# Kernel tuning notes

Measured on AMD Instinct MI355X. Metric: run time of the kernel, lower is better.

Reference implementation:

```python
import jax, jax.numpy as jnp
import numpy as np

T_IN, T_OUT = 16, 25          # in_length, out_length
B, K = 4096, 32               # heroes, neighbors per hero
N = B * K                     # total neighbor tracks
ENC, DEC, DYN, EMB = 64, 128, 32, 32


def _lrelu(x):
    return jnp.where(x >= 0, x, 0.1 * x)


def _lstm(x, Wih, Whh, bih, bhh, hidden):
    """PyTorch-convention LSTM (gate order i,f,g,o). x: [T, B, D]. Returns (all_h [T,B,H], last_h [B,H])."""
    z = jnp.zeros((x.shape[1], hidden), x.dtype)

    def step(carry, xt):
        h, c = carry
        g = xt @ Wih.T + bih + h @ Whh.T + bhh
        i, f, gg, o = jnp.split(g, 4, axis=-1)
        c = jax.nn.sigmoid(f) * c + jax.nn.sigmoid(i) * jnp.tanh(gg)
        h = jax.nn.sigmoid(o) * jnp.tanh(c)
        return (h, c), h

    (h, c), hs = jax.lax.scan(step, (z, z), x)
    return hs, h


def setup_inputs() -> dict:
    key = jax.random.key(0)
    ks = jax.random.split(key, 20)
    p = lambda k, s: jax.random.normal(k, s, jnp.float32) * 0.1
    return {
        "hist": jax.random.normal(ks[0], (T_IN, B, 2), jnp.float32),
        "nbrs": jax.random.normal(ks[1], (T_IN, N, 2), jnp.float32),
        "Wip": p(ks[2], (EMB, 2)), "bip": p(ks[3], (EMB,)),
        "Wih_e": p(ks[4], (4 * ENC, EMB)), "Whh_e": p(ks[5], (4 * ENC, ENC)),
        "bih_e": p(ks[6], (4 * ENC,)), "bhh_e": p(ks[7], (4 * ENC,)),
        "Wdyn": p(ks[8], (DYN, ENC)), "bdyn": p(ks[9], (DYN,)),
        "Wnbr": p(ks[10], (ENC, 2 * T_IN)), "bnbr": p(ks[11], (ENC,)),
        "Wih_d": p(ks[12], (4 * DEC, 2 * DYN)), "Whh_d": p(ks[13], (4 * DEC, DEC)),
        "bih_d": p(ks[14], (4 * DEC,)), "bhh_d": p(ks[15], (4 * DEC,)),
        "Wop": p(ks[16], (2, DEC)), "bop": p(ks[17], (2,)),
        # index_division flattened: neighbor j belongs to hero segment_ids[j] (sorted, K per hero)
        "segment_ids": jnp.repeat(jnp.arange(B, dtype=jnp.int32), K),
    }


def reference(hist, nbrs, Wip, bip, Wih_e, Whh_e, bih_e, bhh_e, Wdyn, bdyn,
              Wnbr, bnbr, Wih_d, Whh_d, bih_d, bhh_d, Wop, bop, segment_ids):
    # --- encode ego history ---
    emb = _lrelu(hist @ Wip.T + bip)                       # [T,B,EMB]
    _, h_enc = _lstm(emb, Wih_e, Whh_e, bih_e, bhh_e, ENC)  # [B,ENC]
    hist_e = _lrelu(h_enc @ Wdyn.T + bdyn)                 # [B,DYN]

    # --- relative neighbor tracks + ragged segment-max pooling ---
    relative = hist[:, segment_ids, :] - nbrs              # [T,N,2]  (hero_repeated gather)
    rela = jnp.transpose(relative, (1, 0, 2)).reshape(N, 2 * T_IN)  # permute(1,0,2).view(-1,2*in_length)
    rela_enc = _lrelu(rela @ Wnbr.T + bnbr)                # [N,ENC]
    scene = jax.ops.segment_max(rela_enc, segment_ids, num_segments=B)  # fused per-group max
    scene = _lrelu(scene @ Wdyn.T + bdyn)                  # [B,DYN]

    # --- decode ---
    enc = jnp.concatenate([hist_e, scene], axis=1)         # [B,2*DYN]
    dec_in = jnp.broadcast_to(enc, (T_OUT, B, 2 * DYN))    # unsqueeze(0).repeat(out_length,1,1)
    h_dec, _ = _lstm(dec_in, Wih_d, Whh_d, bih_d, bhh_d, DEC)  # [T_OUT,B,DEC]
    fut = h_dec @ Wop.T + bop                              # [T_OUT,B,2]
    # outputActivation: with 2 output dims (muX,muY only) it is the identity
    return fut
```

## Files before the change

kernel.cpp:

```cpp
#include <hip/hip_runtime.h>
#include <hip/hip_bf16.h>

#define T_IN   16
#define T_OUT  25
#define BHERO  4096
#define K_NBR  32
#define N_NBR  (BHERO * K_NBR)
#define ENC    64
#define DEC    128
#define DYN    32
#define EMB    32

#define EROW   104
#define DROW   136
#define RROW   40
#define SLABE  (16 * EROW * 2)
#define SLABD  (16 * DROW * 2)

#define OFF_RELA   56576
#define OFF_PMAX   97536
#define OFF_ENC    113152
#define OFF_WOP    117504
#define OFF_WIP    118528
#define OFF_BIP    118784
#define OFF_BOP    118912
#define LDS_TOTAL  118928

#define L2E 1.44269504f

typedef __attribute__((ext_vector_type(8))) short bf16x8;
typedef __attribute__((ext_vector_type(4))) float f32x4;

__device__ __forceinline__ float lrelu(float x) { return x >= 0.f ? x : 0.1f * x; }
__device__ __forceinline__ float rcpf(float x)  { return __builtin_amdgcn_rcpf(x); }
__device__ __forceinline__ float ex2(float x)   { return __builtin_amdgcn_exp2f(x); }
__device__ __forceinline__ float sigm2(float x) { return rcpf(1.f + ex2(-x)); }
__device__ __forceinline__ float tanh2(float x) { return fmaf(2.f, rcpf(1.f + ex2(-x)), -1.f); }
__device__ __forceinline__ float tanhc(float c) {
    return fmaf(2.f, rcpf(1.f + ex2(-2.f * L2E * c)), -1.f);
}
__device__ __forceinline__ short f2bf(float x) {
    __hip_bfloat16 b = __float2bfloat16(x);
    short s; __builtin_memcpy(&s, &b, 2); return s;
}
__device__ __forceinline__ unsigned pk2(float lo, float hi) {
    __hip_bfloat162 p = __float22bfloat162_rn(make_float2(lo, hi));
    unsigned u; __builtin_memcpy(&u, &p, 4); return u;
}
__device__ __forceinline__ bf16x8 mk_frag(float4 f0, float4 f1) {
    uint4 v = { pk2(f0.x, f0.y), pk2(f0.z, f0.w), pk2(f1.x, f1.y), pk2(f1.z, f1.w) };
    bf16x8 r; __builtin_memcpy(&r, &v, 16); return r;
}
__device__ __forceinline__ bf16x8 mk_frag_s(float4 f0, float4 f1, float s) {
    uint4 v = { pk2(f0.x*s, f0.y*s), pk2(f0.z*s, f0.w*s), pk2(f1.x*s, f1.y*s), pk2(f1.z*s, f1.w*s) };
    bf16x8 r; __builtin_memcpy(&r, &v, 16); return r;
}
__device__ __forceinline__ float bf2f(short s) {
    return __uint_as_float(((unsigned)(unsigned short)s) << 16);
}

__global__ __launch_bounds__(512, 2) void highway_fused(
    const float* __restrict__ hist,  const float* __restrict__ nbrs,
    const float* __restrict__ Wip,   const float* __restrict__ bip,
    const float* __restrict__ WihE,  const float* __restrict__ WhhE,
    const float* __restrict__ bihE,  const float* __restrict__ bhhE,
    const float* __restrict__ Wdyn,  const float* __restrict__ bdyn,
    const float* __restrict__ Wnbr,  const float* __restrict__ bnbr,
    const float* __restrict__ WihD,  const float* __restrict__ WhhD,
    const float* __restrict__ bihD,  const float* __restrict__ bhhD,
    const float* __restrict__ Wop,   const float* __restrict__ bop,
    const int*   __restrict__ seg,
    float* __restrict__ fut)
{
    __shared__ __align__(16) char lds_raw[LDS_TOTAL];
    auto slab   = (short (*)[16][EROW])  lds_raw;
    auto rela   = (short (*)[RROW])     (lds_raw + OFF_RELA);
    auto pmax   = (float (*)[ENC])      (lds_raw + OFF_PMAX);
    auto hist_s = (short (*)[16][DROW])  lds_raw;
    auto enc_s  = (float (*)[68])       (lds_raw + OFF_ENC);
    auto wop_s  = (float (*)[DEC])      (lds_raw + OFF_WOP);
    auto wip_s  = (float (*)[2])        (lds_raw + OFF_WIP);
    auto bip_s  = (float*)              (lds_raw + OFF_BIP);
    auto bop_s  = (float*)              (lds_raw + OFF_BOP);

    const int b0  = blockIdx.x * 16;
    const int n0  = blockIdx.x * 512;
    const int tid = threadIdx.x;
    const int w = tid >> 6, l = tid & 63, r = l & 15, lg = l >> 4;

    if (tid < EMB) {
        wip_s[tid][0] = Wip[2 * tid];
        wip_s[tid][1] = Wip[2 * tid + 1];
        bip_s[tid]    = bip[tid];
    }
    if (tid < 2 * DEC) wop_s[tid >> 7][tid & 127] = Wop[tid];
    if (tid < 2)       bop_s[tid] = bop[tid];
    for (int i = tid; i < 16 * ENC; i += 512) slab[0][i >> 6][32 + (i & 63)] = 0;

    bf16x8 BfE[4][3];
    float  biasE[4];
    bf16x8 BfN[2];
    float  biasn[2] = {0.f, 0.f};
    if (tid < 256) {
        #pragma unroll
        for (int j = 0; j < 4; ++j) {
            const float sj  = (j == 2) ? (2.f * L2E) : L2E;
            const int   col = j * ENC + w * 16 + r;
            biasE[j] = (bihE[col] + bhhE[col]) * sj;
            #pragma unroll
            for (int c = 0; c < 3; ++c) {
                const float* src = (c == 0) ? (WihE + (size_t)col * EMB + 8 * lg)
                                            : (WhhE + (size_t)col * ENC + (c - 1) * 32 + 8 * lg);
                BfE[j][c] = mk_frag_s(*(const float4*)src, *(const float4*)(src + 4), sj);
            }
        }
    } else {
        const int i = w - 4;
        const int ct0 = (i & 1) * 2;
        #pragma unroll
        for (int cc2 = 0; cc2 < 2; ++cc2) {
            const int col = (ct0 + cc2) * 16 + r;
            biasn[cc2] = bnbr[col];
            const float* src = Wnbr + (size_t)col * (2 * T_IN) + 8 * lg;
            BfN[cc2] = mk_frag(*(const float4*)src, *(const float4*)(src + 4));
        }
    }
    __syncthreads();

    if (tid < 256) {
        const int t = tid >> 4, m = tid & 15;
        float2 hv = *(const float2*)&hist[((size_t)t * BHERO + b0 + m) * 2];
        #pragma unroll
        for (int jb = 0; jb < 4; ++jb) {
            float e[8];
            #pragma unroll
            for (int q = 0; q < 8; ++q) {
                int j = jb * 8 + q;
                e[q] = lrelu(hv.x * wip_s[j][0] + hv.y * wip_s[j][1] + bip_s[j]);
            }
            uint4 v = { pk2(e[0],e[1]), pk2(e[2],e[3]), pk2(e[4],e[5]), pk2(e[6],e[7]) };
            __builtin_memcpy(&slab[t][m][jb * 8], &v, 16);
        }
    } else {
        const int x = tid - 256;
        const int n  = x & 31;
        const int ts = x >> 5;
        const int hb = seg[n0 + n];
        float2 h0 = *(const float2*)&hist[((size_t)ts * BHERO + hb) * 2];
        float2 v0 = *(const float2*)&nbrs[((size_t)ts * N_NBR + n0 + n) * 2];
        float2 h1 = *(const float2*)&hist[((size_t)(ts + 8) * BHERO + hb) * 2];
        float2 v1 = *(const float2*)&nbrs[((size_t)(ts + 8) * N_NBR + n0 + n) * 2];
        unsigned* dst = (unsigned*)&rela[n][0];
        dst[ts]     = pk2(h0.x - v0.x, h0.y - v0.y);
        dst[ts + 8] = pk2(h1.x - v1.x, h1.y - v1.y);
    }
    f32x4 cstE = {0.f, 0.f, 0.f, 0.f};
    __syncthreads();

    {
        const char* rbase = lds_raw + (size_t)r * (EROW * 2);
        char*       wbase = lds_raw + SLABE + (size_t)(4 * lg) * (EROW * 2) + (size_t)(32 + w * 16 + r) * 2;
        const int   x = tid - 256;
        #pragma unroll 1
        for (int t = 0; t < T_IN; ++t) {
            if (tid < 256) {
                const short* rp = (const short*)rbase;
                bf16x8 a0 = *(const bf16x8*)(rp + (0 + lg) * 8);
                bf16x8 a1 = *(const bf16x8*)(rp + (4 + lg) * 8);
                bf16x8 a2 = *(const bf16x8*)(rp + (8 + lg) * 8);
                f32x4 acc[4];
                #pragma unroll
                for (int j = 0; j < 4; ++j) {
                    f32x4 aA = (f32x4){biasE[j], biasE[j], biasE[j], biasE[j]};
                    f32x4 aB = (f32x4){0.f, 0.f, 0.f, 0.f};
                    aA = __builtin_amdgcn_mfma_f32_16x16x32_bf16(a0, BfE[j][0], aA, 0, 0, 0);
                    aB = __builtin_amdgcn_mfma_f32_16x16x32_bf16(a1, BfE[j][1], aB, 0, 0, 0);
                    aA = __builtin_amdgcn_mfma_f32_16x16x32_bf16(a2, BfE[j][2], aA, 0, 0, 0);
                    acc[j] = aA + aB;
                }
                float hq[4];
                #pragma unroll
                for (int q = 0; q < 4; ++q) {
                    float ii = sigm2(acc[0][q]);
                    float ff = sigm2(acc[1][q]);
                    float gg = tanh2(acc[2][q]);
                    float oo = sigm2(acc[3][q]);
                    float cc = fmaf(ff, cstE[q], ii * gg);
                    cstE[q] = cc;
                    hq[q] = oo * tanhc(cc);
                }
                unsigned u01 = pk2(hq[0], hq[1]), u23 = pk2(hq[2], hq[3]);
                short* wp = (short*)wbase;
                wp[0 * EROW] = (short)u01; wp[1 * EROW] = (short)(u01 >> 16);
                wp[2 * EROW] = (short)u23; wp[3 * EROW] = (short)(u23 >> 16);
            } else {
                if (t < T_IN - 1) {
                    const int n  = 32 * (t + 1) + (x & 31);
                    const int ts = x >> 5;
                    const int hb = seg[n0 + n];
                    float2 h0 = *(const float2*)&hist[((size_t)ts * BHERO + hb) * 2];
                    float2 v0 = *(const float2*)&nbrs[((size_t)ts * N_NBR + n0 + n) * 2];
                    float2 h1 = *(const float2*)&hist[((size_t)(ts + 8) * BHERO + hb) * 2];
                    float2 v1 = *(const float2*)&nbrs[((size_t)(ts + 8) * N_NBR + n0 + n) * 2];
                    unsigned* dst = (unsigned*)&rela[n][0];
                    dst[ts]     = pk2(h0.x - v0.x, h0.y - v0.y);
                    dst[ts + 8] = pk2(h1.x - v1.x, h1.y - v1.y);
                }
                const int i  = w - 4;
                const int rt = 2 * t + (i >> 1);
                const int ct0 = (i & 1) * 2;
                bf16x8 a = *(const bf16x8*)&rela[rt * 16 + r][8 * lg];
                #pragma unroll
                for (int cc2 = 0; cc2 < 2; ++cc2) {
                    f32x4 acc = {biasn[cc2], biasn[cc2], biasn[cc2], biasn[cc2]};
                    acc = __builtin_amdgcn_mfma_f32_16x16x32_bf16(a, BfN[cc2], acc, 0, 0, 0);
                    float m4 = fmaxf(fmaxf(acc[0], acc[1]), fmaxf(acc[2], acc[3]));
                    m4 = fmaxf(m4, __shfl_xor(m4, 16));
                    m4 = fmaxf(m4, __shfl_xor(m4, 32));
                    if (l < 16) pmax[rt][(ct0 + cc2) * 16 + r] = m4;
                }
            }
            __syncthreads();
            rbase += SLABE; wbase += SLABE;
        }
    }

    #pragma unroll
    for (int it = 0; it < 2; ++it) {
        const int s = tid + 512 * it;
        const int m = s >> 6, col = s & 63;
        const float* wd = Wdyn + (size_t)(col & 31) * ENC;
        float a = bdyn[col & 31];
        if (col < 32) {
            const short* hp = &slab[T_IN][m][32];
            #pragma unroll
            for (int kb = 0; kb < 8; ++kb) {
                bf16x8 hv = *(const bf16x8*)(hp + kb * 8);
                #pragma unroll
                for (int e = 0; e < 8; ++e)
                    a = fmaf(bf2f(hv[e]), wd[kb * 8 + e], a);
            }
        } else {
            #pragma unroll
            for (int kb = 0; kb < 16; ++kb) {
                float4 p0 = *(const float4*)&pmax[2 * m][kb * 4];
                float4 p1 = *(const float4*)&pmax[2 * m + 1][kb * 4];
                a = fmaf(lrelu(fmaxf(p0.x, p1.x)), wd[kb * 4 + 0], a);
                a = fmaf(lrelu(fmaxf(p0.y, p1.y)), wd[kb * 4 + 1], a);
                a = fmaf(lrelu(fmaxf(p0.z, p1.z)), wd[kb * 4 + 2], a);
                a = fmaf(lrelu(fmaxf(p0.w, p1.w)), wd[kb * 4 + 3], a);
            }
        }
        enc_s[m][col] = lrelu(a);
    }
    for (int i = tid; i < 16 * DROW; i += 512) ((short*)hist_s)[i] = 0;
    __syncthreads();

    const int u0 = w * 16;
    bf16x8 BfD[4][4];
    float  biasD[4];
    float  sjD[4];
    #pragma unroll
    for (int j = 0; j < 4; ++j) {
        const float sj  = (j == 2) ? (2.f * L2E) : L2E;
        const int   col = j * DEC + u0 + r;
        sjD[j]   = sj;
        biasD[j] = (bihD[col] + bhhD[col]) * sj;
        #pragma unroll
        for (int c = 0; c < 4; ++c) {
            const float* src = WhhD + (size_t)col * DEC + c * 32 + 8 * lg;
            BfD[j][c] = mk_frag_s(*(const float4*)src, *(const float4*)(src + 4), sj);
        }
    }
    f32x4 xwf[4];
    {
        bf16x8 aE[2];
        #pragma unroll
        for (int c = 0; c < 2; ++c) {
            float4 f0 = *(const float4*)&enc_s[r][c * 32 + 8 * lg];
            float4 f1 = *(const float4*)&enc_s[r][c * 32 + 8 * lg + 4];
            aE[c] = mk_frag(f0, f1);
        }
        #pragma unroll
        for (int j = 0; j < 4; ++j) {
            const int col = j * DEC + u0 + r;
            f32x4 a = {biasD[j], biasD[j], biasD[j], biasD[j]};
            #pragma unroll
            for (int c = 0; c < 2; ++c) {
                const float* src = WihD + (size_t)col * (2 * DYN) + c * 32 + 8 * lg;
                a = __builtin_amdgcn_mfma_f32_16x16x32_bf16(
                        aE[c], mk_frag_s(*(const float4*)src, *(const float4*)(src + 4), sjD[j]),
                        a, 0, 0, 0);
            }
            xwf[j] = a;
        }
    }

    f32x4 cst = {0.f, 0.f, 0.f, 0.f};
    {
        const char* rbase = lds_raw + (size_t)r * (DROW * 2);
        char*       wbase = lds_raw + SLABD + (size_t)(4 * lg) * (DROW * 2) + (size_t)(u0 + r) * 2;
        #pragma unroll 1
        for (int t = 0; t < T_OUT; ++t) {
            const short* rp = (const short*)rbase;
            bf16x8 a_[4];
            #pragma unroll
            for (int c = 0; c < 4; ++c)
                a_[c] = *(const bf16x8*)(rp + (4 * c + lg) * 8);
            f32x4 acc[4];
            #pragma unroll
            for (int j = 0; j < 4; ++j) {
                f32x4 aA = xwf[j];
                f32x4 aB = (f32x4){0.f, 0.f, 0.f, 0.f};
                aA = __builtin_amdgcn_mfma_f32_16x16x32_bf16(a_[0], BfD[j][0], aA, 0, 0, 0);
                aB = __builtin_amdgcn_mfma_f32_16x16x32_bf16(a_[1], BfD[j][1], aB, 0, 0, 0);
                aA = __builtin_amdgcn_mfma_f32_16x16x32_bf16(a_[2], BfD[j][2], aA, 0, 0, 0);
                aB = __builtin_amdgcn_mfma_f32_16x16x32_bf16(a_[3], BfD[j][3], aB, 0, 0, 0);
                acc[j] = aA + aB;
            }
            float hq[4];
            #pragma unroll
            for (int q = 0; q < 4; ++q) {
                float ii = sigm2(acc[0][q]);
                float ff = sigm2(acc[1][q]);
                float gg = tanh2(acc[2][q]);
                float oo = sigm2(acc[3][q]);
                float cc = fmaf(ff, cst[q], ii * gg);
                cst[q] = cc;
                hq[q] = oo * tanhc(cc);
            }
            unsigned u01 = pk2(hq[0], hq[1]), u23 = pk2(hq[2], hq[3]);
            short* wp = (short*)wbase;
            wp[0 * DROW] = (short)u01; wp[1 * DROW] = (short)(u01 >> 16);
            wp[2 * DROW] = (short)u23; wp[3 * DROW] = (short)(u23 >> 16);
            __syncthreads();
            rbase += SLABD; wbase += SLABD;
        }
    }

    if (tid < T_OUT * 16) {
        const int t = tid >> 4, m = tid & 15;
        const short* hp = &hist_s[t + 1][m][0];
        float o0 = bop_s[0], o1 = bop_s[1];
        #pragma unroll
        for (int ub = 0; ub < DEC / 8; ++ub) {
            bf16x8 hv = *(const bf16x8*)(hp + ub * 8);
            #pragma unroll
            for (int e = 0; e < 8; ++e) {
                float h = bf2f(hv[e]);
                o0 = fmaf(h, wop_s[0][ub * 8 + e], o0);
                o1 = fmaf(h, wop_s[1][ub * 8 + e], o1);
            }
        }
        *(float2*)(fut + ((size_t)t * BHERO + b0 + m) * 2) = make_float2(o0, o1);
    }
}

extern "C" void kernel_launch(void* const* d_in, const int* in_sizes, int n_in,
                              void* d_out, int out_size, void* d_ws, size_t ws_size,
                              hipStream_t stream) {
    (void)d_ws; (void)ws_size; (void)in_sizes; (void)n_in; (void)out_size;
    const float* hist  = (const float*)d_in[0];
    const float* nbrs  = (const float*)d_in[1];
    const float* Wip   = (const float*)d_in[2];
    const float* bip   = (const float*)d_in[3];
    const float* Wih_e = (const float*)d_in[4];
    const float* Whh_e = (const float*)d_in[5];
    const float* bih_e = (const float*)d_in[6];
    const float* bhh_e = (const float*)d_in[7];
    const float* Wdyn  = (const float*)d_in[8];
    const float* bdyn  = (const float*)d_in[9];
    const float* Wnbr  = (const float*)d_in[10];
    const float* bnbr  = (const float*)d_in[11];
    const float* Wih_d = (const float*)d_in[12];
    const float* Whh_d = (const float*)d_in[13];
    const float* bih_d = (const float*)d_in[14];
    const float* bhh_d = (const float*)d_in[15];
    const float* Wop   = (const float*)d_in[16];
    const float* bop   = (const float*)d_in[17];
    const int*   seg   = (const int*)d_in[18];
    float* fut = (float*)d_out;

    hipLaunchKernelGGL(highway_fused, dim3(BHERO / 16), dim3(512), 0, stream,
                       hist, nbrs, Wip, bip, Wih_e, Whh_e, bih_e, bhh_e, Wdyn, bdyn,
                       Wnbr, bnbr, Wih_d, Whh_d, bih_d, bhh_d, Wop, bop, seg, fut);
}
```

Before: 63.58 us.

## Software-pipeline neighbor loads with double-buffered rela and lighter LDS-only barriers

Neighbor relative-track loads are now issued two timesteps ahead into registers, and the segment id three steps ahead. The rela LDS buffer shrinks to a two-slot ring indexed by timestep parity, so global load latency overlaps the encoder LSTM steps instead of stalling each iteration. __syncthreads is replaced by an inline asm that waits only on lgkmcnt before s_barrier, so barriers no longer wait for outstanding global loads. This costs extra registers, and correctness depends on the parity buffer not being overwritten before it is read.

```diff
diff --git a/kernel.cpp b/kernel.cpp
--- a/kernel.cpp
+++ b/kernel.cpp
@@ -39,10 +39,6 @@
 __device__ __forceinline__ float tanhc(float c) {
     return fmaf(2.f, rcpf(1.f + ex2(-2.f * L2E * c)), -1.f);
 }
-__device__ __forceinline__ short f2bf(float x) {
-    __hip_bfloat16 b = __float2bfloat16(x);
-    short s; __builtin_memcpy(&s, &b, 2); return s;
-}
 __device__ __forceinline__ unsigned pk2(float lo, float hi) {
     __hip_bfloat162 p = __float22bfloat162_rn(make_float2(lo, hi));
     unsigned u; __builtin_memcpy(&u, &p, 4); return u;
@@ -57,6 +53,9 @@
 }
 __device__ __forceinline__ float bf2f(short s) {
     return __uint_as_float(((unsigned)(unsigned short)s) << 16);
+}
+__device__ __forceinline__ void bar_lgkm() {
+    asm volatile("s_waitcnt lgkmcnt(0)\n\ts_barrier" ::: "memory");
 }
 
 __global__ __launch_bounds__(512, 2) void highway_fused(
@@ -74,7 +73,7 @@
 {
     __shared__ __align__(16) char lds_raw[LDS_TOTAL];
     auto slab   = (short (*)[16][EROW])  lds_raw;
-    auto rela   = (short (*)[RROW])     (lds_raw + OFF_RELA);
+    auto rela2  = (short (*)[32][RROW]) (lds_raw + OFF_RELA);
     auto pmax   = (float (*)[ENC])      (lds_raw + OFF_PMAX);
     auto hist_s = (short (*)[16][DROW])  lds_raw;
     auto enc_s  = (float (*)[68])       (lds_raw + OFF_ENC);
@@ -125,8 +124,10 @@
             BfN[cc2] = mk_frag(*(const float4*)src, *(const float4*)(src + 4));
         }
     }
-    __syncthreads();
-
+    bar_lgkm();
+
+    float2 c_h0, c_v0, c_h1, c_v1;
+    int    sg_c = 0;
     if (tid < 256) {
         const int t = tid >> 4, m = tid & 15;
         float2 hv = *(const float2*)&hist[((size_t)t * BHERO + b0 + m) * 2];
@@ -142,25 +143,38 @@
             __builtin_memcpy(&slab[t][m][jb * 8], &v, 16);
         }
     } else {
-        const int x = tid - 256;
-        const int n  = x & 31;
-        const int ts = x >> 5;
-        const int hb = seg[n0 + n];
-        float2 h0 = *(const float2*)&hist[((size_t)ts * BHERO + hb) * 2];
-        float2 v0 = *(const float2*)&nbrs[((size_t)ts * N_NBR + n0 + n) * 2];
-        float2 h1 = *(const float2*)&hist[((size_t)(ts + 8) * BHERO + hb) * 2];
-        float2 v1 = *(const float2*)&nbrs[((size_t)(ts + 8) * N_NBR + n0 + n) * 2];
-        unsigned* dst = (unsigned*)&rela[n][0];
-        dst[ts]     = pk2(h0.x - v0.x, h0.y - v0.y);
-        dst[ts + 8] = pk2(h1.x - v1.x, h1.y - v1.y);
+        const int x    = tid - 256;
+        const int nloc = x & 31;
+        const int ts   = x >> 5;
+        {
+            const int hb = seg[n0 + nloc];
+            float2 h0 = *(const float2*)&hist[((size_t)ts * BHERO + hb) * 2];
+            float2 v0 = *(const float2*)&nbrs[((size_t)ts * N_NBR + n0 + nloc) * 2];
+            float2 h1 = *(const float2*)&hist[((size_t)(ts + 8) * BHERO + hb) * 2];
+            float2 v1 = *(const float2*)&nbrs[((size_t)(ts + 8) * N_NBR + n0 + nloc) * 2];
+            unsigned* dst = (unsigned*)&rela2[0][nloc][0];
+            dst[ts]     = pk2(h0.x - v0.x, h0.y - v0.y);
+            dst[ts + 8] = pk2(h1.x - v1.x, h1.y - v1.y);
+        }
+        {
+            const int n  = 32 + nloc;
+            const int hb = seg[n0 + n];
+            c_h0 = *(const float2*)&hist[((size_t)ts * BHERO + hb) * 2];
+            c_v0 = *(const float2*)&nbrs[((size_t)ts * N_NBR + n0 + n) * 2];
+            c_h1 = *(const float2*)&hist[((size_t)(ts + 8) * BHERO + hb) * 2];
+            c_v1 = *(const float2*)&nbrs[((size_t)(ts + 8) * N_NBR + n0 + n) * 2];
+        }
+        sg_c = seg[n0 + 64 + nloc];
     }
     f32x4 cstE = {0.f, 0.f, 0.f, 0.f};
-    __syncthreads();
+    bar_lgkm();
 
     {
         const char* rbase = lds_raw + (size_t)r * (EROW * 2);
         char*       wbase = lds_raw + SLABE + (size_t)(4 * lg) * (EROW * 2) + (size_t)(32 + w * 16 + r) * 2;
-        const int   x = tid - 256;
+        const int   x    = tid - 256;
+        const int   nloc = x & 31;
+        const int   ts   = x >> 5;
         #pragma unroll 1
         for (int t = 0; t < T_IN; ++t) {
             if (tid < 256) {
@@ -194,22 +208,26 @@
                 wp[0 * EROW] = (short)u01; wp[1 * EROW] = (short)(u01 >> 16);
                 wp[2 * EROW] = (short)u23; wp[3 * EROW] = (short)(u23 >> 16);
             } else {
+                float2 n_h0, n_v0, n_h1, n_v1;
+                int    sg_n = 0;
+                if (t < T_IN - 2) {
+                    const int n  = 32 * (t + 2) + nloc;
+                    const int hb = sg_c;
+                    n_h0 = *(const float2*)&hist[((size_t)ts * BHERO + hb) * 2];
+                    n_v0 = *(const float2*)&nbrs[((size_t)ts * N_NBR + n0 + n) * 2];
+                    n_h1 = *(const float2*)&hist[((size_t)(ts + 8) * BHERO + hb) * 2];
+                    n_v1 = *(const float2*)&nbrs[((size_t)(ts + 8) * N_NBR + n0 + n) * 2];
+                }
+                if (t < T_IN - 3) sg_n = seg[n0 + 32 * (t + 3) + nloc];
                 if (t < T_IN - 1) {
-                    const int n  = 32 * (t + 1) + (x & 31);
-                    const int ts = x >> 5;
-                    const int hb = seg[n0 + n];
-                    float2 h0 = *(const float2*)&hist[((size_t)ts * BHERO + hb) * 2];
-                    float2 v0 = *(const float2*)&nbrs[((size_t)ts * N_NBR + n0 + n) * 2];
-                    float2 h1 = *(const float2*)&hist[((size_t)(ts + 8) * BHERO + hb) * 2];
-                    float2 v1 = *(const float2*)&nbrs[((size_t)(ts + 8) * N_NBR + n0 + n) * 2];
-                    unsigned* dst = (unsigned*)&rela[n][0];
-                    dst[ts]     = pk2(h0.x - v0.x, h0.y - v0.y);
-                    dst[ts + 8] = pk2(h1.x - v1.x, h1.y - v1.y);
+                    unsigned* dst = (unsigned*)&rela2[(t + 1) & 1][nloc][0];
+                    dst[ts]     = pk2(c_h0.x - c_v0.x, c_h0.y - c_v0.y);
+                    dst[ts + 8] = pk2(c_h1.x - c_v1.x, c_h1.y - c_v1.y);
                 }
-                const int i  = w - 4;
-                const int rt = 2 * t + (i >> 1);
+                const int i   = w - 4;
+                const int lrt = i >> 1;
                 const int ct0 = (i & 1) * 2;
-                bf16x8 a = *(const bf16x8*)&rela[rt * 16 + r][8 * lg];
+                bf16x8 a = *(const bf16x8*)&rela2[t & 1][lrt * 16 + r][8 * lg];
                 #pragma unroll
                 for (int cc2 = 0; cc2 < 2; ++cc2) {
                     f32x4 acc = {biasn[cc2], biasn[cc2], biasn[cc2], biasn[cc2]};
@@ -217,10 +235,12 @@
                     float m4 = fmaxf(fmaxf(acc[0], acc[1]), fmaxf(acc[2], acc[3]));
                     m4 = fmaxf(m4, __shfl_xor(m4, 16));
                     m4 = fmaxf(m4, __shfl_xor(m4, 32));
-                    if (l < 16) pmax[rt][(ct0 + cc2) * 16 + r] = m4;
+                    if (l < 16) pmax[2 * t + lrt][(ct0 + cc2) * 16 + r] = m4;
                 }
-            }
-            __syncthreads();
+                c_h0 = n_h0; c_v0 = n_v0; c_h1 = n_h1; c_v1 = n_v1;
+                sg_c = sg_n;
+            }
+            bar_lgkm();
             rbase += SLABE; wbase += SLABE;
         }
     }
@@ -254,7 +274,7 @@
         enc_s[m][col] = lrelu(a);
     }
     for (int i = tid; i < 16 * DROW; i += 512) ((short*)hist_s)[i] = 0;
-    __syncthreads();
+    bar_lgkm();
 
     const int u0 = w * 16;
     bf16x8 BfD[4][4];
@@ -333,7 +353,7 @@
             short* wp = (short*)wbase;
             wp[0 * DROW] = (short)u01; wp[1 * DROW] = (short)(u01 >> 16);
             wp[2 * DROW] = (short)u23; wp[3 * DROW] = (short)(u23 >> 16);
-            __syncthreads();
+            bar_lgkm();
             rbase += SLABD; wbase += SLABD;
         }
     }
```

Result: no change. 64.21 us (+1.0%).

## Halve heroes per block to 8 with 256 threads and ring-buffered LDS state

Applied to the files above, without the earlier changes.

Each block now handles 8 heroes with 256 threads instead of 16 heroes with 512, which doubles the grid to 512 blocks. The 16-row MFMA tiles are filled by duplicating each hero's rows, so half of the matrix work is redundant. Each wave computes two unit slices and keeps only its own. Full per-timestep LDS slabs are replaced by double-buffered rings, cutting LDS use from about 119KB to 66KB so more blocks can be resident per CU. Barriers now use a custom lgkmcnt wait plus s_barrier. The trade is more grid parallelism and occupancy against duplicated MFMA work and more registers per thread.

```diff
diff --git a/kernel.cpp b/kernel.cpp
--- a/kernel.cpp
+++ b/kernel.cpp
@@ -10,21 +10,22 @@
 #define DEC    128
 #define DYN    32
 #define EMB    32
-
-#define EROW   104
+#define HEROES 8
+
 #define DROW   136
+#define HROW   72
+#define EMROW  40
 #define RROW   40
-#define SLABE  (16 * EROW * 2)
-#define SLABD  (16 * DROW * 2)
-
-#define OFF_RELA   56576
-#define OFF_PMAX   97536
-#define OFF_ENC    113152
-#define OFF_WOP    117504
-#define OFF_WIP    118528
-#define OFF_BIP    118784
-#define OFF_BOP    118912
-#define LDS_TOTAL  118928
+
+#define OFF_HRING  20480
+#define OFF_RELA   25088
+#define OFF_PMAX   27648
+#define OFF_ENC    59904
+#define OFF_WOP    64256
+#define OFF_WIP    65280
+#define OFF_BIP    65536
+#define OFF_BOP    65664
+#define LDS_TOTAL  65680
 
 #define L2E 1.44269504f
 
@@ -58,8 +59,11 @@
 __device__ __forceinline__ float bf2f(short s) {
     return __uint_as_float(((unsigned)(unsigned short)s) << 16);
 }
-
-__global__ __launch_bounds__(512, 2) void highway_fused(
+__device__ __forceinline__ void bar_lgkm() {
+    asm volatile("s_waitcnt lgkmcnt(0)\n\ts_barrier" ::: "memory");
+}
+
+__global__ __launch_bounds__(256, 2) void highway_fused(
     const float* __restrict__ hist,  const float* __restrict__ nbrs,
     const float* __restrict__ Wip,   const float* __restrict__ bip,
     const float* __restrict__ WihE,  const float* __restrict__ WhhE,
@@ -73,50 +77,58 @@
     float* __restrict__ fut)
 {
     __shared__ __align__(16) char lds_raw[LDS_TOTAL];
-    auto slab   = (short (*)[16][EROW])  lds_raw;
-    auto rela   = (short (*)[RROW])     (lds_raw + OFF_RELA);
-    auto pmax   = (float (*)[ENC])      (lds_raw + OFF_PMAX);
-    auto hist_s = (short (*)[16][DROW])  lds_raw;
-    auto enc_s  = (float (*)[68])       (lds_raw + OFF_ENC);
-    auto wop_s  = (float (*)[DEC])      (lds_raw + OFF_WOP);
-    auto wip_s  = (float (*)[2])        (lds_raw + OFF_WIP);
-    auto bip_s  = (float*)              (lds_raw + OFF_BIP);
-    auto bop_s  = (float*)              (lds_raw + OFF_BOP);
-
-    const int b0  = blockIdx.x * 16;
-    const int n0  = blockIdx.x * 512;
+    auto ring   = (short (*)[16][DROW])   lds_raw;
+    auto hhist  = (short (*)[HEROES][DEC])(lds_raw + 8704);
+    auto embs   = (short (*)[16][EMROW])  lds_raw;
+    auto hring  = (short (*)[16][HROW])  (lds_raw + OFF_HRING);
+    auto rela   = (short (*)[16][RROW])  (lds_raw + OFF_RELA);
+    auto pmax   = (float (*)[ENC])       (lds_raw + OFF_PMAX);
+    auto enc_s  = (float (*)[68])        (lds_raw + OFF_ENC);
+    auto wop_s  = (float (*)[DEC])       (lds_raw + OFF_WOP);
+    auto wip_s  = (float (*)[2])         (lds_raw + OFF_WIP);
+    auto bip_s  = (float*)               (lds_raw + OFF_BIP);
+    auto bop_s  = (float*)               (lds_raw + OFF_BOP);
+
+    const int b0  = blockIdx.x * HEROES;
+    const int n0  = blockIdx.x * (HEROES * K_NBR);
     const int tid = threadIdx.x;
     const int w = tid >> 6, l = tid & 63, r = l & 15, lg = l >> 4;
+    const int ubsel = lg >> 1;
+    const int hgrp  = (lg & 1) * 4;
+    const int unit  = 32 * w + 16 * ubsel + r;
 
     if (tid < EMB) {
         wip_s[tid][0] = Wip[2 * tid];
         wip_s[tid][1] = Wip[2 * tid + 1];
         bip_s[tid]    = bip[tid];
     }
-    if (tid < 2 * DEC) wop_s[tid >> 7][tid & 127] = Wop[tid];
-    if (tid < 2)       bop_s[tid] = bop[tid];
-    for (int i = tid; i < 16 * ENC; i += 512) slab[0][i >> 6][32 + (i & 63)] = 0;
-
-    bf16x8 BfE[4][3];
-    float  biasE[4];
+    wop_s[tid >> 7][tid & 127] = Wop[tid];
+    if (tid < 2) bop_s[tid] = bop[tid];
+    for (int i = tid; i < 16 * HROW; i += 256) ((short*)hring[0])[i] = 0;
+    bar_lgkm();
+
+    bf16x8 BfE[2][4][3];
+    float  biasE[2][4];
     bf16x8 BfN[2];
     float  biasn[2] = {0.f, 0.f};
-    if (tid < 256) {
-        #pragma unroll
-        for (int j = 0; j < 4; ++j) {
-            const float sj  = (j == 2) ? (2.f * L2E) : L2E;
-            const int   col = j * ENC + w * 16 + r;
-            biasE[j] = (bihE[col] + bhhE[col]) * sj;
-            #pragma unroll
-            for (int c = 0; c < 3; ++c) {
-                const float* src = (c == 0) ? (WihE + (size_t)col * EMB + 8 * lg)
-                                            : (WhhE + (size_t)col * ENC + (c - 1) * 32 + 8 * lg);
-                BfE[j][c] = mk_frag_s(*(const float4*)src, *(const float4*)(src + 4), sj);
+    if (tid < 128) {
+        #pragma unroll
+        for (int ub = 0; ub < 2; ++ub) {
+            #pragma unroll
+            for (int j = 0; j < 4; ++j) {
+                const float sj  = (j == 2) ? (2.f * L2E) : L2E;
+                const int   col = j * ENC + 32 * w + 16 * ub + r;
+                biasE[ub][j] = (bihE[col] + bhhE[col]) * sj;
+                #pragma unroll
+                for (int c = 0; c < 3; ++c) {
+                    const float* src = (c == 0) ? (WihE + (size_t)col * EMB + 8 * lg)
+                                                : (WhhE + (size_t)col * ENC + (c - 1) * 32 + 8 * lg);
+                    BfE[ub][j][c] = mk_frag_s(*(const float4*)src, *(const float4*)(src + 4), sj);
+                }
             }
         }
     } else {
-        const int i = w - 4;
-        const int ct0 = (i & 1) * 2;
+        const int ct0 = 2 * (w - 2);
         #pragma unroll
         for (int cc2 = 0; cc2 < 2; ++cc2) {
             const int col = (ct0 + cc2) * 16 + r;
@@ -125,114 +137,114 @@
             BfN[cc2] = mk_frag(*(const float4*)src, *(const float4*)(src + 4));
         }
     }
-    __syncthreads();
-
-    if (tid < 256) {
-        const int t = tid >> 4, m = tid & 15;
+    {
+        const int task = tid >> 1;
+        const int t = task >> 3, m = task & 7;
+        const int j0 = (tid & 1) * 16;
         float2 hv = *(const float2*)&hist[((size_t)t * BHERO + b0 + m) * 2];
         #pragma unroll
-        for (int jb = 0; jb < 4; ++jb) {
+        for (int jb = 0; jb < 2; ++jb) {
             float e[8];
             #pragma unroll
             for (int q = 0; q < 8; ++q) {
-                int j = jb * 8 + q;
+                int j = j0 + jb * 8 + q;
                 e[q] = lrelu(hv.x * wip_s[j][0] + hv.y * wip_s[j][1] + bip_s[j]);
             }
             uint4 v = { pk2(e[0],e[1]), pk2(e[2],e[3]), pk2(e[4],e[5]), pk2(e[6],e[7]) };
-            __builtin_memcpy(&slab[t][m][jb * 8], &v, 16);
-        }
-    } else {
-        const int x = tid - 256;
-        const int n  = x & 31;
-        const int ts = x >> 5;
+            __builtin_memcpy(&embs[t][m][j0 + jb * 8], &v, 16);
+            __builtin_memcpy(&embs[t][m + 8][j0 + jb * 8], &v, 16);
+        }
+    }
+    if (tid >= 128) {
+        const int x  = tid - 128;
+        const int n  = x & 15;
+        const int ts = x >> 4;
         const int hb = seg[n0 + n];
         float2 h0 = *(const float2*)&hist[((size_t)ts * BHERO + hb) * 2];
         float2 v0 = *(const float2*)&nbrs[((size_t)ts * N_NBR + n0 + n) * 2];
         float2 h1 = *(const float2*)&hist[((size_t)(ts + 8) * BHERO + hb) * 2];
         float2 v1 = *(const float2*)&nbrs[((size_t)(ts + 8) * N_NBR + n0 + n) * 2];
-        unsigned* dst = (unsigned*)&rela[n][0];
+        unsigned* dst = (unsigned*)&rela[0][n][0];
         dst[ts]     = pk2(h0.x - v0.x, h0.y - v0.y);
         dst[ts + 8] = pk2(h1.x - v1.x, h1.y - v1.y);
     }
     f32x4 cstE = {0.f, 0.f, 0.f, 0.f};
-    __syncthreads();
-
-    {
-        const char* rbase = lds_raw + (size_t)r * (EROW * 2);
-        char*       wbase = lds_raw + SLABE + (size_t)(4 * lg) * (EROW * 2) + (size_t)(32 + w * 16 + r) * 2;
-        const int   x = tid - 256;
-        #pragma unroll 1
-        for (int t = 0; t < T_IN; ++t) {
-            if (tid < 256) {
-                const short* rp = (const short*)rbase;
-                bf16x8 a0 = *(const bf16x8*)(rp + (0 + lg) * 8);
-                bf16x8 a1 = *(const bf16x8*)(rp + (4 + lg) * 8);
-                bf16x8 a2 = *(const bf16x8*)(rp + (8 + lg) * 8);
-                f32x4 acc[4];
+    bar_lgkm();
+
+    #pragma unroll 1
+    for (int t = 0; t < T_IN; ++t) {
+        const int cur = t & 1, nxt = cur ^ 1;
+        if (tid < 128) {
+            bf16x8 a0 = *(const bf16x8*)&embs[t][r][8 * lg];
+            bf16x8 a1 = *(const bf16x8*)&hring[cur][r][8 * lg];
+            bf16x8 a2 = *(const bf16x8*)&hring[cur][r][32 + 8 * lg];
+            f32x4 acc[2][4];
+            #pragma unroll
+            for (int ub = 0; ub < 2; ++ub) {
                 #pragma unroll
                 for (int j = 0; j < 4; ++j) {
-                    f32x4 aA = (f32x4){biasE[j], biasE[j], biasE[j], biasE[j]};
+                    f32x4 aA = (f32x4){biasE[ub][j], biasE[ub][j], biasE[ub][j], biasE[ub][j]};
                     f32x4 aB = (f32x4){0.f, 0.f, 0.f, 0.f};
-                    aA = __builtin_amdgcn_mfma_f32_16x16x32_bf16(a0, BfE[j][0], aA, 0, 0, 0);
-                    aB = __builtin_amdgcn_mfma_f32_16x16x32_bf16(a1, BfE[j][1], aB, 0, 0, 0);
-                    aA = __builtin_amdgcn_mfma_f32_16x16x32_bf16(a2, BfE[j][2], aA, 0, 0, 0);
-                    acc[j] = aA + aB;
+                    aA = __builtin_amdgcn_mfma_f32_16x16x32_bf16(a0, BfE[ub][j][0], aA, 0, 0, 0);
+                    aB = __builtin_amdgcn_mfma_f32_16x16x32_bf16(a1, BfE[ub][j][1], aB, 0, 0, 0);
+                    aA = __builtin_amdgcn_mfma_f32_16x16x32_bf16(a2, BfE[ub][j][2], aA, 0, 0, 0);
+                    acc[ub][j] = aA + aB;
                 }
-                float hq[4];
-                #pragma unroll
-                for (int q = 0; q < 4; ++q) {
-                    float ii = sigm2(acc[0][q]);
-                    float ff = sigm2(acc[1][q]);
-                    float gg = tanh2(acc[2][q]);
-                    float oo = sigm2(acc[3][q]);
-                    float cc = fmaf(ff, cstE[q], ii * gg);
-                    cstE[q] = cc;
-                    hq[q] = oo * tanhc(cc);
-                }
-                unsigned u01 = pk2(hq[0], hq[1]), u23 = pk2(hq[2], hq[3]);
-                short* wp = (short*)wbase;
-                wp[0 * EROW] = (short)u01; wp[1 * EROW] = (short)(u01 >> 16);
-                wp[2 * EROW] = (short)u23; wp[3 * EROW] = (short)(u23 >> 16);
-            } else {
-                if (t < T_IN - 1) {
-                    const int n  = 32 * (t + 1) + (x & 31);
-                    const int ts = x >> 5;
-                    const int hb = seg[n0 + n];
-                    float2 h0 = *(const float2*)&hist[((size_t)ts * BHERO + hb) * 2];
-                    float2 v0 = *(const float2*)&nbrs[((size_t)ts * N_NBR + n0 + n) * 2];
-                    float2 h1 = *(const float2*)&hist[((size_t)(ts + 8) * BHERO + hb) * 2];
-                    float2 v1 = *(const float2*)&nbrs[((size_t)(ts + 8) * N_NBR + n0 + n) * 2];
-                    unsigned* dst = (unsigned*)&rela[n][0];
-                    dst[ts]     = pk2(h0.x - v0.x, h0.y - v0.y);
-                    dst[ts + 8] = pk2(h1.x - v1.x, h1.y - v1.y);
-                }
-                const int i  = w - 4;
-                const int rt = 2 * t + (i >> 1);
-                const int ct0 = (i & 1) * 2;
-                bf16x8 a = *(const bf16x8*)&rela[rt * 16 + r][8 * lg];
-                #pragma unroll
-                for (int cc2 = 0; cc2 < 2; ++cc2) {
-                    f32x4 acc = {biasn[cc2], biasn[cc2], biasn[cc2], biasn[cc2]};
-                    acc = __builtin_amdgcn_mfma_f32_16x16x32_bf16(a, BfN[cc2], acc, 0, 0, 0);
-                    float m4 = fmaxf(fmaxf(acc[0], acc[1]), fmaxf(acc[2], acc[3]));
-                    m4 = fmaxf(m4, __shfl_xor(m4, 16));
-                    m4 = fmaxf(m4, __shfl_xor(m4, 32));
-                    if (l < 16) pmax[rt][(ct0 + cc2) * 16 + r] = m4;
-                }
-            }
-            __syncthreads();
-            rbase += SLABE; wbase += SLABE;
-        }
+            }
+            f32x4 g0 = (ubsel == 0) ? acc[0][0] : acc[1][0];
+            f32x4 g1 = (ubsel == 0) ? acc[0][1] : acc[1][1];
+            f32x4 g2 = (ubsel == 0) ? acc[0][2] : acc[1][2];
+            f32x4 g3 = (ubsel == 0) ? acc[0][3] : acc[1][3];
+            const int ue = 32 * w + 16 * ubsel + r;
+            #pragma unroll
+            for (int q = 0; q < 4; ++q) {
+                float ii = sigm2(g0[q]);
+                float ff = sigm2(g1[q]);
+                float gg = tanh2(g2[q]);
+                float oo = sigm2(g3[q]);
+                float cc = fmaf(ff, cstE[q], ii * gg);
+                cstE[q] = cc;
+                short hb16 = f2bf(oo * tanhc(cc));
+                hring[nxt][hgrp + q][ue]     = hb16;
+                hring[nxt][hgrp + q + 8][ue] = hb16;
+            }
+        } else {
+            const int x = tid - 128;
+            if (t < T_IN - 1) {
+                const int n  = 16 * (t + 1) + (x & 15);
+                const int ts = x >> 4;
+                const int hb = seg[n0 + n];
+                float2 h0 = *(const float2*)&hist[((size_t)ts * BHERO + hb) * 2];
+                float2 v0 = *(const float2*)&nbrs[((size_t)ts * N_NBR + n0 + n) * 2];
+                float2 h1 = *(const float2*)&hist[((size_t)(ts + 8) * BHERO + hb) * 2];
+                float2 v1 = *(const float2*)&nbrs[((size_t)(ts + 8) * N_NBR + n0 + n) * 2];
+                unsigned* dst = (unsigned*)&rela[(t + 1) & 1][x & 15][0];
+                dst[ts]     = pk2(h0.x - v0.x, h0.y - v0.y);
+                dst[ts + 8] = pk2(h1.x - v1.x, h1.y - v1.y);
+            }
+            const int ct0 = 2 * (w - 2);
+            bf16x8 a = *(const bf16x8*)&rela[t & 1][r][8 * lg];
+            #pragma unroll
+            for (int cc2 = 0; cc2 < 2; ++cc2) {
+                f32x4 acc = {biasn[cc2], biasn[cc2], biasn[cc2], biasn[cc2]};
+                acc = __builtin_amdgcn_mfma_f32_16x16x32_bf16(a, BfN[cc2], acc, 0, 0, 0);
+                float m4 = fmaxf(fmaxf(acc[0], acc[1]), fmaxf(acc[2], acc[3]));
+                m4 = fmaxf(m4, __shfl_xor(m4, 16));
+                m4 = fmaxf(m4, __shfl_xor(m4, 32));
+                if (l < 16) pmax[t][(ct0 + cc2) * 16 + r] = m4;
+            }
+        }
+        bar_lgkm();
     }
 
     #pragma unroll
     for (int it = 0; it < 2; ++it) {
-        const int s = tid + 512 * it;
+        const int s = tid + 256 * it;
         const int m = s >> 6, col = s & 63;
         const float* wd = Wdyn + (size_t)(col & 31) * ENC;
         float a = bdyn[col & 31];
         if (col < 32) {
-            const short* hp = &slab[T_IN][m][32];
+            const short* hp = &hring[T_IN & 1 ^ 0][m][0];
             #pragma unroll
             for (int kb = 0; kb < 8; ++kb) {
                 bf16x8 hv = *(const bf16x8*)(hp + kb * 8);
@@ -251,28 +263,30 @@
                 a = fmaf(lrelu(fmaxf(p0.w, p1.w)), wd[kb * 4 + 3], a);
             }
         }
-        enc_s[m][col] = lrelu(a);
-    }
-    for (int i = tid; i < 16 * DROW; i += 512) ((short*)hist_s)[i] = 0;
-    __syncthreads();
-
-    const int u0 = w * 16;
-    bf16x8 BfD[4][4];
-    float  biasD[4];
-    float  sjD[4];
+        float av = lrelu(a);
+        enc_s[m][col]     = av;
+        enc_s[m + 8][col] = av;
+    }
+    for (int i = tid; i < 16 * DROW; i += 256) ((short*)ring[0])[i] = 0;
+    bar_lgkm();
+
+    bf16x8 BfD[2][4][4];
+    float  biasD[2][4];
     #pragma unroll
-    for (int j = 0; j < 4; ++j) {
-        const float sj  = (j == 2) ? (2.f * L2E) : L2E;
-        const int   col = j * DEC + u0 + r;
-        sjD[j]   = sj;
-        biasD[j] = (bihD[col] + bhhD[col]) * sj;
-        #pragma unroll
-        for (int c = 0; c < 4; ++c) {
-            const float* src = WhhD + (size_t)col * DEC + c * 32 + 8 * lg;
-            BfD[j][c] = mk_frag_s(*(const float4*)src, *(const float4*)(src + 4), sj);
-        }
-    }
-    f32x4 xwf[4];
+    for (int ub = 0; ub < 2; ++ub) {
+        #pragma unroll
+        for (int j = 0; j < 4; ++j) {
+            const float sj  = (j == 2) ? (2.f * L2E) : L2E;
+            const int   col = j * DEC + 32 * w + 16 * ub + r;
+            biasD[ub][j] = (bihD[col] + bhhD[col]) * sj;
+            #pragma unroll
+            for (int c = 0; c < 4; ++c) {
+                const float* src = WhhD + (size_t)col * DEC + c * 32 + 8 * lg;
+                BfD[ub][j][c] = mk_frag_s(*(const float4*)src, *(const float4*)(src + 4), sj);
+            }
+        }
+    }
+    f32x4 xwf[2][4];
     {
         bf16x8 aE[2];
         #pragma unroll
@@ -282,65 +296,70 @@
             aE[c] = mk_frag(f0, f1);
         }
         #pragma unroll
-        for (int j = 0; j < 4; ++j) {
-            const int col = j * DEC + u0 + r;
-            f32x4 a = {biasD[j], biasD[j], biasD[j], biasD[j]};
-            #pragma unroll
-            for (int c = 0; c < 2; ++c) {
-                const float* src = WihD + (size_t)col * (2 * DYN) + c * 32 + 8 * lg;
-                a = __builtin_amdgcn_mfma_f32_16x16x32_bf16(
-                        aE[c], mk_frag_s(*(const float4*)src, *(const float4*)(src + 4), sjD[j]),
-                        a, 0, 0, 0);
-            }
-            xwf[j] = a;
+        for (int ub = 0; ub < 2; ++ub) {
+            #pragma unroll
+            for (int j = 0; j < 4; ++j) {
+                const float sj  = (j == 2) ? (2.f * L2E) : L2E;
+                const int   col = j * DEC + 32 * w + 16 * ub + r;
+                f32x4 a = {biasD[ub][j], biasD[ub][j], biasD[ub][j], biasD[ub][j]};
+                #pragma unroll
+                for (int c = 0; c < 2; ++c) {
+                    const float* src = WihD + (size_t)col * (2 * DYN) + c * 32 + 8 * lg;
+                    a = __builtin_amdgcn_mfma_f32_16x16x32_bf16(
+                            aE[c], mk_frag_s(*(const float4*)src, *(const float4*)(src + 4), sj),
+                            a, 0, 0, 0);
+                }
+                xwf[ub][j] = a;
+            }
         }
     }
 
     f32x4 cst = {0.f, 0.f, 0.f, 0.f};
-    {
-        const char* rbase = lds_raw + (size_t)r * (DROW * 2);
-        char*       wbase = lds_raw + SLABD + (size_t)(4 * lg) * (DROW * 2) + (size_t)(u0 + r) * 2;
-        #pragma unroll 1
-        for (int t = 0; t < T_OUT; ++t) {
-            const short* rp = (const short*)rbase;
-            bf16x8 a_[4];
-            #pragma unroll
-            for (int c = 0; c < 4; ++c)
-                a_[c] = *(const bf16x8*)(rp + (4 * c + lg) * 8);
-            f32x4 acc[4];
+    #pragma unroll 1
+    for (int t = 0; t < T_OUT; ++t) {
+        const int cur = t & 1, nxt = cur ^ 1;
+        const short* rp = &ring[cur][r][0];
+        bf16x8 a_[4];
+        #pragma unroll
+        for (int c = 0; c < 4; ++c)
+            a_[c] = *(const bf16x8*)(rp + (4 * c + lg) * 8);
+        f32x4 acc[2][4];
+        #pragma unroll
+        for (int ub = 0; ub < 2; ++ub) {
             #pragma unroll
             for (int j = 0; j < 4; ++j) {
-                f32x4 aA = xwf[j];
+                f32x4 aA = xwf[ub][j];
                 f32x4 aB = (f32x4){0.f, 0.f, 0.f, 0.f};
-                aA = __builtin_amdgcn_mfma_f32_16x16x32_bf16(a_[0], BfD[j][0], aA, 0, 0, 0);
-                aB = __builtin_amdgcn_mfma_f32_16x16x32_bf16(a_[1], BfD[j][1], aB, 0, 0, 0);
-                aA = __builtin_amdgcn_mfma_f32_16x16x32_bf16(a_[2], BfD[j][2], aA, 0, 0, 0);
-                aB = __builtin_amdgcn_mfma_f32_16x16x32_bf16(a_[3], BfD[j][3], aB, 0, 0, 0);
-                acc[j] = aA + aB;
-            }
-            float hq[4];
-            #pragma unroll
-            for (int q = 0; q < 4; ++q) {
-                float ii = sigm2(acc[0][q]);
-                float ff = sigm2(acc[1][q]);
-                float gg = tanh2(acc[2][q]);
-                float oo = sigm2(acc[3][q]);
-                float cc = fmaf(ff, cst[q], ii * gg);
-                cst[q] = cc;
-                hq[q] = oo * tanhc(cc);
-            }
-            unsigned u01 = pk2(hq[0], hq[1]), u23 = pk2(hq[2], hq[3]);
-            short* wp = (short*)wbase;
-            wp[0 * DROW] = (short)u01; wp[1 * DROW] = (short)(u01 >> 16);
-            wp[2 * DROW] = (short)u23; wp[3 * DROW] = (short)(u23 >> 16);
-            __syncthreads();
-            rbase += SLABD; wbase += SLABD;
-        }
-    }
-
-    if (tid < T_OUT * 16) {
-        const int t = tid >> 4, m = tid & 15;
-        const short* hp = &hist_s[t + 1][m][0];
+                aA = __builtin_amdgcn_mfma_f32_16x16x32_bf16(a_[0], BfD[ub][j][0], aA, 0, 0, 0);
+                aB = __builtin_amdgcn_mfma_f32_16x16x32_bf16(a_[1], BfD[ub][j][1], aB, 0, 0, 0);
+                aA = __builtin_amdgcn_mfma_f32_16x16x32_bf16(a_[2], BfD[ub][j][2], aA, 0, 0, 0);
+                aB = __builtin_amdgcn_mfma_f32_16x16x32_bf16(a_[3], BfD[ub][j][3], aB, 0, 0, 0);
+                acc[ub][j] = aA + aB;
+            }
+        }
+        f32x4 g0 = (ubsel == 0) ? acc[0][0] : acc[1][0];
+        f32x4 g1 = (ubsel == 0) ? acc[0][1] : acc[1][1];
+        f32x4 g2 = (ubsel == 0) ? acc[0][2] : acc[1][2];
+        f32x4 g3 = (ubsel == 0) ? acc[0][3] : acc[1][3];
+        #pragma unroll
+        for (int q = 0; q < 4; ++q) {
+            float ii = sigm2(g0[q]);
+            float ff = sigm2(g1[q]);
+            float gg = tanh2(g2[q]);
+            float oo = sigm2(g3[q]);
+            float cc = fmaf(ff, cst[q], ii * gg);
+            cst[q] = cc;
+            short hb16 = f2bf(oo * tanhc(cc));
+            ring[nxt][hgrp + q][unit]     = hb16;
+            ring[nxt][hgrp + q + 8][unit] = hb16;
+            hhist[t][hgrp + q][unit]      = hb16;
+        }
+        bar_lgkm();
+    }
+
+    if (tid < T_OUT * HEROES) {
+        const int t = tid >> 3, m = tid & 7;
+        const short* hp = &hhist[t][m][0];
         float o0 = bop_s[0], o1 = bop_s[1];
         #pragma unroll
         for (int ub = 0; ub < DEC / 8; ++ub) {
@@ -381,7 +400,7 @@
     const int*   seg   = (const int*)d_in[18];
     float* fut = (float*)d_out;
 
-    hipLaunchKernelGGL(highway_fused, dim3(BHERO / 16), dim3(512), 0, stream,
+    hipLaunchKernelGGL(highway_fused, dim3(BHERO / HEROES), dim3(256), 0, stream,
                        hist, nbrs, Wip, bip, Wih_e, Whh_e, bih_e, bhh_e, Wdyn, bdyn,
                        Wnbr, bnbr, Wih_d, Whh_d, bih_d, bhh_d, Wop, bop, seg, fut);
 }
```

Result: slower. 79.81 us (+25.5%).
